# Kernel optimization log

Hardware: AMD Instinct MI355X
Metric: run time of the kernel (lower is better)

## Reference

```python
import jax, jax.numpy as jnp
import numpy as np

N = 50000          # num nodes
E = 1_600_000      # num edges (avg degree 32)
F = 512            # node_dim
C = 64             # num_clusters
O = 256            # output_dim


def setup_inputs() -> dict:
    key = jax.random.key(0)
    ks = jax.random.split(key, 9)
    lim_p = 1.0 / np.sqrt(F)
    inp = {
        "x": jax.random.normal(ks[0], (N, F), dtype=jnp.float32),
        "edge_index": jax.random.randint(ks[1], (2, E), 0, N, dtype=jnp.int64),
        "batch": jnp.zeros((N,), dtype=jnp.int64),
        # gnn_pool: Linear(F, C)
        "Wp": jax.random.uniform(ks[2], (F, C), jnp.float32, -lim_p, lim_p),
        "bp": jax.random.uniform(ks[3], (C,), jnp.float32, -lim_p, lim_p),
        # gnn_embed: Linear(F, F)
        "We": jax.random.uniform(ks[4], (F, F), jnp.float32, -lim_p, lim_p),
        "be": jax.random.uniform(ks[5], (F,), jnp.float32, -lim_p, lim_p),
        # projection: Linear(F, O)
        "Wo": jax.random.uniform(ks[6], (F, O), jnp.float32, -lim_p, lim_p),
        "bo": jax.random.uniform(ks[7], (O,), jnp.float32, -lim_p, lim_p),
    }
    return inp


def reference(x, edge_index, batch, Wp, bp, We, be, Wo, bo):
    # s = softmax(gnn_pool(x), -1): soft cluster assignments  [N, C]
    s = jax.nn.softmax(x @ Wp + bp, axis=-1)
    # h = gnn_embed(x)  [N, F]
    h = x @ We + be
    # dense_diff_pool pooled features: out = s^T h  -> [C, F]
    # (out_adj = s^T A s and the link/entropy reg are computed by the
    #  original but discarded; they do not affect the returned output.)
    pooled = jnp.einsum("nc,nf->cf", s, h)
    # PyG dense_diff_pool unsqueezes 2D inputs to batch dim 1 -> [1, C, F]
    out = pooled[None] @ Wo + bo  # [1, C, O]
    return out
```

## Files before the change

### kernel.cpp

```cpp
#include <hip/hip_runtime.h>
#include <hip/hip_bf16.h>

typedef __attribute__((ext_vector_type(8))) short short8;
typedef __attribute__((ext_vector_type(4))) float floatx4;
typedef __attribute__((ext_vector_type(4))) unsigned uint4v;
typedef __attribute__((ext_vector_type(4))) unsigned short ushort4v;

#define FDIM 512
#define CDIM 64
#define ODIM 256
#define TR   32
#define XSF  516
#define STS 40
#define MAXP 256
#define RSW(r) ((((r) >> 3) & 3) << 2)

__device__ __forceinline__ ushort f2bf(float f) {
    union { float f; unsigned u; } v; v.f = f;
    unsigned r = v.u + 0x7FFFu + ((v.u >> 16) & 1u);
    return (ushort)(r >> 16);
}
__device__ __forceinline__ float bf2f(unsigned hi16) {
    union { unsigned u; float f; } v; v.u = hi16 << 16; return v.f;
}

__device__ __forceinline__ void gld16(const float* g, float* lds_base) {
    __builtin_amdgcn_global_load_lds(
        (const __attribute__((address_space(1))) unsigned int*)(const void*)g,
        (__attribute__((address_space(3))) unsigned int*)(void*)lds_base,
        16, 0, 0);
}

__global__ __launch_bounds__(256) void kWpT(const float* __restrict__ Wp,
                                            ushort* __restrict__ WpT) {
    int g = blockIdx.x * 256 + threadIdx.x;
    int f = g >> 6, c = g & 63;
    WpT[c * FDIM + f] = f2bf(Wp[f * CDIM + c]);
}

__global__ __launch_bounds__(512, 2) void kFused(
        const float* __restrict__ x, const ushort* __restrict__ WpT,
        const float* __restrict__ bp, ushort* __restrict__ part,
        float* __restrict__ cpart, int N, int nTiles, int P) {
    __shared__ float  xsf[2][TR * XSF + 16];
    __shared__ ushort sT[CDIM][STS];
    __shared__ float  red1[TR][4];
    __shared__ float  red2[TR][4];
    __shared__ float  cred[CDIM][2];

    const int t    = threadIdx.x;
    const int w    = t >> 6;
    const int lane = t & 63;
    const int l16  = lane & 15;
    const int q    = lane >> 4;
    const int ci   = w & 3;
    const int rg   = w >> 2;

    floatx4 acc[4][4];
#pragma unroll
    for (int mt = 0; mt < 4; ++mt)
#pragma unroll
        for (int nt = 0; nt < 4; ++nt) acc[mt][nt] = (floatx4){0.f, 0.f, 0.f, 0.f};
    float csp[4] = {0.f, 0.f, 0.f, 0.f};

    float bpv[4];
#pragma unroll
    for (int reg = 0; reg < 4; ++reg) bpv[reg] = bp[16 * ci + 4 * q + reg];

    const ushort* wb = WpT + (size_t)(16 * ci + l16) * FDIM + q * 8;
    short8 af[4][4];
#pragma unroll
    for (int kb = 0; kb < 4; ++kb)
#pragma unroll
        for (int ki = 0; ki < 4; ++ki)
            af[kb][ki] = *(const short8*)(wb + kb * 128 + ki * 32);

    auto stage = [&](int tile, float* xb) {
        const int row0s = tile * TR;
#pragma unroll
        for (int i = 0; i < 8; ++i) {
            const int c0 = w * 8 + i;
            const int r  = c0 >> 1;
            const int h  = c0 & 1;
            float* lb = xb + r * XSF + RSW(r) + h * 256;
            if (row0s + r < N) {
                const float* g = x + (size_t)(row0s + r) * FDIM + h * 256 + lane * 4;
                gld16(g, lb);
            } else {
                *(floatx4*)(lb + lane * 4) = (floatx4){0.f, 0.f, 0.f, 0.f};
            }
        }
    };

    stage(blockIdx.x, xsf[0]);
    __syncthreads();

    int it = 0;
    for (int tile = blockIdx.x; tile < nTiles; tile += P, ++it) {
        float* xb = xsf[it & 1];
        if (tile + P < nTiles) stage(tile + P, xsf[(it & 1) ^ 1]);

        const int row0 = tile * TR;

        floatx4 acc1 = (floatx4){0.f, 0.f, 0.f, 0.f};
        const int prow = 16 * rg + l16;
        const float* xr = xb + prow * XSF + RSW(prow);
#pragma unroll
        for (int kb = 0; kb < 4; ++kb) {
#pragma unroll
            for (int ki = 0; ki < 4; ++ki) {
                const int off = kb * 128 + ki * 32 + q * 8;
                floatx4 u0 = *(const floatx4*)(xr + off);
                floatx4 u1 = *(const floatx4*)(xr + off + 4);
                short8 b;
                b[0] = (short)f2bf(u0[0]); b[1] = (short)f2bf(u0[1]);
                b[2] = (short)f2bf(u0[2]); b[3] = (short)f2bf(u0[3]);
                b[4] = (short)f2bf(u1[0]); b[5] = (short)f2bf(u1[1]);
                b[6] = (short)f2bf(u1[2]); b[7] = (short)f2bf(u1[3]);
                acc1 = __builtin_amdgcn_mfma_f32_16x16x32_bf16(af[kb][ki], b, acc1, 0, 0, 0);
            }
        }

        const int row = prow;
        float lg[4];
#pragma unroll
        for (int reg = 0; reg < 4; ++reg) lg[reg] = acc1[reg] + bpv[reg];
        float m = fmaxf(fmaxf(lg[0], lg[1]), fmaxf(lg[2], lg[3]));
        m = fmaxf(m, __shfl_xor(m, 16));
        m = fmaxf(m, __shfl_xor(m, 32));
        if (lane < 16) red1[16 * rg + lane][ci] = m;
        __syncthreads();
        const float rmax = fmaxf(fmaxf(red1[row][0], red1[row][1]),
                                 fmaxf(red1[row][2], red1[row][3]));
        float p = 0.f;
#pragma unroll
        for (int reg = 0; reg < 4; ++reg) {
            float e = __expf(lg[reg] - rmax);
            lg[reg] = e; p += e;
        }
        p += __shfl_xor(p, 16);
        p += __shfl_xor(p, 32);
        if (lane < 16) red2[16 * rg + lane][ci] = p;
        __syncthreads();
        const float rsi = 1.0f / (red2[row][0] + red2[row][1] +
                                  red2[row][2] + red2[row][3]);
        const bool valid = (row0 + row) < N;
#pragma unroll
        for (int reg = 0; reg < 4; ++reg) {
            float s = valid ? lg[reg] * rsi : 0.f;
            sT[16 * ci + 4 * q + reg][row] = f2bf(s);
            csp[reg] += s;
        }
        __syncthreads();

        short8 as_[4];
#pragma unroll
        for (int mt = 0; mt < 4; ++mt)
            as_[mt] = *(const short8*)&sT[16 * mt + l16][q * 8];
#pragma unroll
        for (int nt = 0; nt < 4; ++nt) {
            const int f = 64 * w + 16 * nt + l16;
            short8 b;
#pragma unroll
            for (int j = 0; j < 8; ++j)
                b[j] = (short)f2bf(xb[(q * 8 + j) * XSF + 4 * q + f]);
#pragma unroll
            for (int mt = 0; mt < 4; ++mt)
                acc[mt][nt] = __builtin_amdgcn_mfma_f32_16x16x32_bf16(
                    as_[mt], b, acc[mt][nt], 0, 0, 0);
        }

        __syncthreads();
    }

#pragma unroll
    for (int reg = 0; reg < 4; ++reg) {
        float v = csp[reg];
        v += __shfl_xor(v, 1); v += __shfl_xor(v, 2);
        v += __shfl_xor(v, 4); v += __shfl_xor(v, 8);
        if (l16 == 0) cred[16 * ci + 4 * q + reg][rg] = v;
    }
    __syncthreads();
    if (t < 64) cpart[(size_t)blockIdx.x * CDIM + t] = cred[t][0] + cred[t][1];

    ushort* xf = (ushort*)xsf;
#pragma unroll
    for (int mt = 0; mt < 4; ++mt)
#pragma unroll
        for (int nt = 0; nt < 4; ++nt)
#pragma unroll
            for (int reg = 0; reg < 4; ++reg)
                xf[(16 * mt + 4 * q + reg) * FDIM + 64 * w + 16 * nt + l16] =
                    f2bf(acc[mt][nt][reg]);
    __syncthreads();
    const uint4v* src = (const uint4v*)xf;
    uint4v* dst = (uint4v*)(part + (size_t)blockIdx.x * (CDIM * FDIM));
#pragma unroll
    for (int i = 0; i < 8; ++i)
        dst[i * 512 + t] = src[i * 512 + t];
}

__global__ __launch_bounds__(512) void kR(const ushort* __restrict__ part,
                                          const float* __restrict__ cpart,
                                          float* __restrict__ colsum,
                                          float* __restrict__ Mp,
                                          int P, int pch) {
    __shared__ float ws8[8];
    const int c = blockIdx.x, pc = blockIdx.y, t = threadIdx.x;
    const int g  = t >> 7;
    const int f0 = (t & 127) << 2;
    const int p0 = pc * pch, p1 = min(p0 + pch, P);

    float s0 = 0.f, s1 = 0.f, s2 = 0.f, s3 = 0.f;
    for (int p = p0 + g; p < p1; p += 4) {
        const ushort4v v = *(const ushort4v*)(part + (size_t)p * (CDIM * FDIM)
                                              + (size_t)c * FDIM + f0);
        s0 += bf2f((unsigned)v[0]); s1 += bf2f((unsigned)v[1]);
        s2 += bf2f((unsigned)v[2]); s3 += bf2f((unsigned)v[3]);
    }
    floatx4 o = (floatx4){s0, s1, s2, s3};
    *(floatx4*)(Mp + (((size_t)(pc * 4 + g) * CDIM + c) * FDIM + f0)) = o;

    float cv = 0.f;
    {
        int p = p0 + t;
        if (p < p1) cv = cpart[(size_t)p * CDIM + c];
    }
    cv += __shfl_xor(cv, 1);  cv += __shfl_xor(cv, 2);
    cv += __shfl_xor(cv, 4);  cv += __shfl_xor(cv, 8);
    cv += __shfl_xor(cv, 16); cv += __shfl_xor(cv, 32);
    if ((t & 63) == 0) ws8[t >> 6] = cv;
    __syncthreads();
    if (t == 0) {
        float tot = 0.f;
#pragma unroll
        for (int i = 0; i < 8; ++i) tot += ws8[i];
        atomicAdd(colsum + c, tot);
    }
}

__global__ __launch_bounds__(512) void kC(const float* __restrict__ Mp,
                                          const float* __restrict__ colsum,
                                          const float* __restrict__ We,
                                          const float* __restrict__ be,
                                          const float* __restrict__ Wo,
                                          const float* __restrict__ bo,
                                          float* __restrict__ out) {
    __shared__ float Mrow[512];
    __shared__ float pooled[512];
    __shared__ float halves[2][256];
    const int c = blockIdx.x, t = threadIdx.x;

    float sum = 0.f;
#pragma unroll
    for (int pc = 0; pc < 32; ++pc)
        sum += Mp[((size_t)pc * CDIM + c) * FDIM + t];
    Mrow[t] = sum;
    __syncthreads();

    float a = colsum[c] * be[t];
#pragma unroll 16
    for (int k = 0; k < FDIM; ++k)
        a = fmaf(Mrow[k], We[(size_t)k * FDIM + t], a);
    pooled[t] = a;
    __syncthreads();

    const int o = t & 255, h = t >> 8;
    float b = 0.f;
#pragma unroll 16
    for (int kk = 0; kk < 256; ++kk) {
        int k = h * 256 + kk;
        b = fmaf(pooled[k], Wo[(size_t)k * ODIM + o], b);
    }
    halves[h][o] = b;
    __syncthreads();
    if (t < 256)
        out[(size_t)c * ODIM + t] = halves[0][t] + halves[1][t] + bo[t];
}

extern "C" void kernel_launch(void* const* d_in, const int* in_sizes, int n_in,
                              void* d_out, int out_size, void* d_ws, size_t ws_size,
                              hipStream_t stream) {
    const float* x  = (const float*)d_in[0];
    const float* Wp = (const float*)d_in[3];
    const float* bp = (const float*)d_in[4];
    const float* We = (const float*)d_in[5];
    const float* be = (const float*)d_in[6];
    const float* Wo = (const float*)d_in[7];
    const float* bo = (const float*)d_in[8];
    float* out = (float*)d_out;

    const int N = in_sizes[0] / FDIM;
    const int nTiles = (N + TR - 1) / TR;

    char*   wsb    = (char*)d_ws;
    ushort* WpT    = (ushort*)wsb;
    float*  colsum = (float*)(wsb + 65536);
    float*  cpart  = (float*)(wsb + 66560);
    float*  Mp     = (float*)(wsb + 266752);
    const size_t PART_OFF = 4461056;
    ushort* part   = (ushort*)(wsb + PART_OFF);

    size_t avail = (ws_size > PART_OFF + 65536) ? (ws_size - PART_OFF) / 65536 : 1;
    int P = (int)(avail < (size_t)MAXP ? avail : (size_t)MAXP);
    if (P > nTiles) P = nTiles;
    if (P < 1) P = 1;
    const int pch = (P + 7) / 8;

    hipMemsetAsync(colsum, 0, 256, stream);
    kWpT<<<128, 256, 0, stream>>>(Wp, WpT);
    kFused<<<P, 512, 0, stream>>>(x, WpT, bp, part, cpart, N, nTiles, P);
    kR<<<dim3(CDIM, 8), 512, 0, stream>>>(part, cpart, colsum, Mp, P, pch);
    kC<<<CDIM, 512, 0, stream>>>(Mp, colsum, We, be, Wo, bo, out);
}
```

Measured before the change: 223.0 us.

## Stage x tiles as swizzled bf16 in LDS via register prefetch, drop WpT kernel

Replaces the direct global-to-LDS fp32 staging with register prefetch of the next tile. Each element is converted to bf16 once and written into an XOR-swizzled bf16 LDS buffer, so both MFMA phases read bf16 directly instead of converting fp32 twice. The Wp transpose kernel is removed and Wp is gathered and converted inside the fused kernel. The logits MFMA chain is split into two accumulators, and barriers become a lighter LDS-only wait plus s_barrier. The trade-offs are extra registers for prefetched data and strided Wp loads per block.

```diff
diff --git a/kernel.cpp b/kernel.cpp
--- a/kernel.cpp
+++ b/kernel.cpp
@@ -10,10 +10,8 @@
 #define CDIM 64
 #define ODIM 256
 #define TR   32
-#define XSF  516
-#define STS 40
+#define STS  40
 #define MAXP 256
-#define RSW(r) ((((r) >> 3) & 3) << 2)
 
 __device__ __forceinline__ ushort f2bf(float f) {
     union { float f; unsigned u; } v; v.f = f;
@@ -24,28 +22,20 @@
     union { unsigned u; float f; } v; v.u = hi16 << 16; return v.f;
 }
 
-__device__ __forceinline__ void gld16(const float* g, float* lds_base) {
-    __builtin_amdgcn_global_load_lds(
-        (const __attribute__((address_space(1))) unsigned int*)(const void*)g,
-        (__attribute__((address_space(3))) unsigned int*)(void*)lds_base,
-        16, 0, 0);
-}
-
-__global__ __launch_bounds__(256) void kWpT(const float* __restrict__ Wp,
-                                            ushort* __restrict__ WpT) {
-    int g = blockIdx.x * 256 + threadIdx.x;
-    int f = g >> 6, c = g & 63;
-    WpT[c * FDIM + f] = f2bf(Wp[f * CDIM + c]);
-}
+#define LBAR() do {                                            \
+    asm volatile("s_waitcnt lgkmcnt(0)" ::: "memory");         \
+    __builtin_amdgcn_s_barrier();                              \
+    asm volatile("" ::: "memory");                             \
+} while (0)
 
 __global__ __launch_bounds__(512, 2) void kFused(
-        const float* __restrict__ x, const ushort* __restrict__ WpT,
+        const float* __restrict__ x, const float* __restrict__ Wp,
         const float* __restrict__ bp, ushort* __restrict__ part,
         float* __restrict__ cpart, int N, int nTiles, int P) {
-    __shared__ float  xsf[2][TR * XSF + 16];
-    __shared__ ushort sT[CDIM][STS];
-    __shared__ float  red1[TR][4];
-    __shared__ float  red2[TR][4];
+    __shared__ __align__(16) ushort xb2[2][TR * FDIM];
+    __shared__ __align__(16) ushort sT[CDIM][STS];
+    __shared__ __align__(16) float  red1[TR][4];
+    __shared__ __align__(16) float  red2[TR][4];
     __shared__ float  cred[CDIM][2];
 
     const int t    = threadIdx.x;
@@ -67,69 +57,85 @@
 #pragma unroll
     for (int reg = 0; reg < 4; ++reg) bpv[reg] = bp[16 * ci + 4 * q + reg];
 
-    const ushort* wb = WpT + (size_t)(16 * ci + l16) * FDIM + q * 8;
     short8 af[4][4];
-#pragma unroll
-    for (int kb = 0; kb < 4; ++kb)
-#pragma unroll
-        for (int ki = 0; ki < 4; ++ki)
-            af[kb][ki] = *(const short8*)(wb + kb * 128 + ki * 32);
-
-    auto stage = [&](int tile, float* xb) {
+    {
+        const int c = 16 * ci + l16;
+#pragma unroll
+        for (int kb = 0; kb < 4; ++kb)
+#pragma unroll
+            for (int ki = 0; ki < 4; ++ki) {
+                short8 a;
+#pragma unroll
+                for (int j = 0; j < 8; ++j)
+                    a[j] = (short)f2bf(
+                        Wp[(size_t)(kb * 128 + ki * 32 + q * 8 + j) * CDIM + c]);
+                af[kb][ki] = a;
+            }
+    }
+
+    floatx4 st[8];
+    auto issue = [&](int tile) {
         const int row0s = tile * TR;
 #pragma unroll
         for (int i = 0; i < 8; ++i) {
-            const int c0 = w * 8 + i;
-            const int r  = c0 >> 1;
-            const int h  = c0 & 1;
-            float* lb = xb + r * XSF + RSW(r) + h * 256;
-            if (row0s + r < N) {
-                const float* g = x + (size_t)(row0s + r) * FDIM + h * 256 + lane * 4;
-                gld16(g, lb);
-            } else {
-                *(floatx4*)(lb + lane * 4) = (floatx4){0.f, 0.f, 0.f, 0.f};
+            const int g  = i * 512 + t;
+            const int r  = g >> 7;
+            const int f4 = g & 127;
+            int rr = row0s + r;
+            if (rr >= N) rr = N - 1;
+            st[i] = *(const floatx4*)(x + (size_t)rr * FDIM + f4 * 4);
+        }
+    };
+    auto commit = [&](ushort* xb) {
+#pragma unroll
+        for (int i = 0; i < 8; ++i) {
+            const int g  = i * 512 + t;
+            const int r  = g >> 7;
+            const int f0 = (g & 127) << 2;
+            ushort4v v;
+            v[0] = f2bf(st[i][0]); v[1] = f2bf(st[i][1]);
+            v[2] = f2bf(st[i][2]); v[3] = f2bf(st[i][3]);
+            *(ushort4v*)(xb + r * FDIM + (f0 ^ ((r & 7) << 3))) = v;
+        }
+    };
+
+    issue(blockIdx.x);
+    commit(xb2[0]);
+    LBAR();
+
+    int cur = 0;
+    for (int tile = blockIdx.x; tile < nTiles; tile += P) {
+        const int  row0 = tile * TR;
+        const bool pf   = (tile + P) < nTiles;
+        if (pf) issue(tile + P);
+
+        const ushort* xr = &xb2[cur][0];
+
+        const int prow = 16 * rg + l16;
+        const int sw   = (prow & 7) << 3;
+        const ushort* xrow = xr + prow * FDIM;
+        floatx4 a1a = (floatx4){0.f, 0.f, 0.f, 0.f};
+        floatx4 a1b = (floatx4){0.f, 0.f, 0.f, 0.f};
+#pragma unroll
+        for (int kb = 0; kb < 4; ++kb)
+#pragma unroll
+            for (int ki = 0; ki < 4; ++ki) {
+                short8 b = *(const short8*)(xrow + ((kb * 128 + ki * 32 + q * 8) ^ sw));
+                if (kb & 1)
+                    a1b = __builtin_amdgcn_mfma_f32_16x16x32_bf16(af[kb][ki], b, a1b, 0, 0, 0);
+                else
+                    a1a = __builtin_amdgcn_mfma_f32_16x16x32_bf16(af[kb][ki], b, a1a, 0, 0, 0);
             }
-        }
-    };
-
-    stage(blockIdx.x, xsf[0]);
-    __syncthreads();
-
-    int it = 0;
-    for (int tile = blockIdx.x; tile < nTiles; tile += P, ++it) {
-        float* xb = xsf[it & 1];
-        if (tile + P < nTiles) stage(tile + P, xsf[(it & 1) ^ 1]);
-
-        const int row0 = tile * TR;
-
-        floatx4 acc1 = (floatx4){0.f, 0.f, 0.f, 0.f};
-        const int prow = 16 * rg + l16;
-        const float* xr = xb + prow * XSF + RSW(prow);
-#pragma unroll
-        for (int kb = 0; kb < 4; ++kb) {
-#pragma unroll
-            for (int ki = 0; ki < 4; ++ki) {
-                const int off = kb * 128 + ki * 32 + q * 8;
-                floatx4 u0 = *(const floatx4*)(xr + off);
-                floatx4 u1 = *(const floatx4*)(xr + off + 4);
-                short8 b;
-                b[0] = (short)f2bf(u0[0]); b[1] = (short)f2bf(u0[1]);
-                b[2] = (short)f2bf(u0[2]); b[3] = (short)f2bf(u0[3]);
-                b[4] = (short)f2bf(u1[0]); b[5] = (short)f2bf(u1[1]);
-                b[6] = (short)f2bf(u1[2]); b[7] = (short)f2bf(u1[3]);
-                acc1 = __builtin_amdgcn_mfma_f32_16x16x32_bf16(af[kb][ki], b, acc1, 0, 0, 0);
-            }
-        }
 
         const int row = prow;
         float lg[4];
 #pragma unroll
-        for (int reg = 0; reg < 4; ++reg) lg[reg] = acc1[reg] + bpv[reg];
+        for (int reg = 0; reg < 4; ++reg) lg[reg] = a1a[reg] + a1b[reg] + bpv[reg];
         float m = fmaxf(fmaxf(lg[0], lg[1]), fmaxf(lg[2], lg[3]));
         m = fmaxf(m, __shfl_xor(m, 16));
         m = fmaxf(m, __shfl_xor(m, 32));
         if (lane < 16) red1[16 * rg + lane][ci] = m;
-        __syncthreads();
+        LBAR();
         const float rmax = fmaxf(fmaxf(red1[row][0], red1[row][1]),
                                  fmaxf(red1[row][2], red1[row][3]));
         float p = 0.f;
@@ -141,7 +147,7 @@
         p += __shfl_xor(p, 16);
         p += __shfl_xor(p, 32);
         if (lane < 16) red2[16 * rg + lane][ci] = p;
-        __syncthreads();
+        LBAR();
         const float rsi = 1.0f / (red2[row][0] + red2[row][1] +
                                   red2[row][2] + red2[row][3]);
         const bool valid = (row0 + row) < N;
@@ -151,7 +157,7 @@
             sT[16 * ci + 4 * q + reg][row] = f2bf(s);
             csp[reg] += s;
         }
-        __syncthreads();
+        LBAR();
 
         short8 as_[4];
 #pragma unroll
@@ -159,18 +165,20 @@
             as_[mt] = *(const short8*)&sT[16 * mt + l16][q * 8];
 #pragma unroll
         for (int nt = 0; nt < 4; ++nt) {
-            const int f = 64 * w + 16 * nt + l16;
+            const int fc = 64 * w + 16 * nt + l16;
             short8 b;
 #pragma unroll
             for (int j = 0; j < 8; ++j)
-                b[j] = (short)f2bf(xb[(q * 8 + j) * XSF + 4 * q + f]);
+                b[j] = (short)xr[(q * 8 + j) * FDIM + (fc ^ (j << 3))];
 #pragma unroll
             for (int mt = 0; mt < 4; ++mt)
                 acc[mt][nt] = __builtin_amdgcn_mfma_f32_16x16x32_bf16(
                     as_[mt], b, acc[mt][nt], 0, 0, 0);
         }
 
-        __syncthreads();
+        if (pf) commit(xb2[cur ^ 1]);
+        LBAR();
+        cur ^= 1;
     }
 
 #pragma unroll
@@ -183,7 +191,7 @@
     __syncthreads();
     if (t < 64) cpart[(size_t)blockIdx.x * CDIM + t] = cred[t][0] + cred[t][1];
 
-    ushort* xf = (ushort*)xsf;
+    ushort* xf = &xb2[0][0];
 #pragma unroll
     for (int mt = 0; mt < 4; ++mt)
 #pragma unroll
@@ -294,11 +302,10 @@
     const int nTiles = (N + TR - 1) / TR;
 
     char*   wsb    = (char*)d_ws;
-    ushort* WpT    = (ushort*)wsb;
-    float*  colsum = (float*)(wsb + 65536);
-    float*  cpart  = (float*)(wsb + 66560);
-    float*  Mp     = (float*)(wsb + 266752);
-    const size_t PART_OFF = 4461056;
+    float*  colsum = (float*)wsb;
+    float*  cpart  = (float*)(wsb + 1024);
+    float*  Mp     = (float*)(wsb + 66560);
+    const size_t PART_OFF = 4260864;
     ushort* part   = (ushort*)(wsb + PART_OFF);
 
     size_t avail = (ws_size > PART_OFF + 65536) ? (ws_size - PART_OFF) / 65536 : 1;
@@ -308,8 +315,7 @@
     const int pch = (P + 7) / 8;
 
     hipMemsetAsync(colsum, 0, 256, stream);
-    kWpT<<<128, 256, 0, stream>>>(Wp, WpT);
-    kFused<<<P, 512, 0, stream>>>(x, WpT, bp, part, cpart, N, nTiles, P);
+    kFused<<<P, 512, 0, stream>>>(x, Wp, bp, part, cpart, N, nTiles, P);
     kR<<<dim3(CDIM, 8), 512, 0, stream>>>(part, cpart, colsum, Mp, P, pch);
     kC<<<CDIM, 512, 0, stream>>>(Mp, colsum, We, be, Wo, bo, out);
 }
```

New measurement: 220.6 us. No clear change (-1.1%).
